# Kernel tuning notes

Hardware: AMD Instinct MI355X
Metric: run time of the kernel (lower is better)

## Reference

```python
import jax, jax.numpy as jnp
import numpy as np

B, SEQ, I_TSIZE, H, N_LAYERS = 512, 256, 64, 512, 2
E_CONST = 2.7183


def setup_inputs() -> dict:
    key = jax.random.key(0)
    ks = jax.random.split(key, 16)
    feats = jax.random.normal(ks[0], (B, SEQ, I_TSIZE - 1), dtype=jnp.float32)
    dt = jax.random.uniform(ks[1], (B, SEQ, 1), dtype=jnp.float32)  # elapsed time >= 0
    inputs_t = jnp.concatenate([feats, dt], axis=-1)  # [B, SEQ, I_TSIZE]
    i_size = I_TSIZE - 1
    inp = {"inputs_t": inputs_t}
    in_dims = [i_size, H]
    for l in range(N_LAYERS):
        c_inp = in_dims[l]
        s = 1.0 / np.sqrt(c_inp + H)
        inp[f"W{l}"] = jax.random.normal(ks[2 + 4 * l], (4 * H, c_inp + H), dtype=jnp.float32) * s
        inp[f"b{l}"] = jax.random.normal(ks[3 + 4 * l], (4 * H,), dtype=jnp.float32) * s
        sd = 1.0 / np.sqrt(H)
        inp[f"Wd{l}"] = jax.random.normal(ks[4 + 4 * l], (H, H), dtype=jnp.float32) * sd
        inp[f"bd{l}"] = jax.random.normal(ks[5 + 4 * l], (H,), dtype=jnp.float32) * sd
    return inp


def _tlstm_layer(curr_inp, W, b, Wd, bd):
    # curr_inp: [B, SEQ, feat+1] (last channel = dt). Scan over REVERSED time,
    # as in the torch loop `for t_seq in reversed(range(seq_l))`.
    batch = curr_inp.shape[0]
    h0 = jnp.zeros((batch, H), dtype=curr_inp.dtype)
    c0 = jnp.zeros((batch, H), dtype=curr_inp.dtype)

    def step(carry, xt):
        h, c = carry
        x, dt = xt[:, :-1], xt[:, -1:]
        T = 1.0 / jnp.log(dt + E_CONST)          # [B,1], broadcasts over H
        C_ST = jnp.tanh(h @ Wd.T + bd)
        h = h - C_ST + T * C_ST                  # time-decay correction
        z = jnp.concatenate([x, h], axis=1) @ W.T + b  # [B, 4H]
        ci, cf, co, cg = jnp.split(z, 4, axis=1)
        c_next = jax.nn.sigmoid(cf) * c + jax.nn.sigmoid(ci) * jnp.tanh(cg)
        h_next = jax.nn.sigmoid(co) * jnp.tanh(c_next)
        return (h_next, c_next), h_next

    xs = jnp.swapaxes(curr_inp[:, ::-1, :], 0, 1)  # [SEQ, B, feat+1], reversed time
    (h, c), hs = jax.lax.scan(step, (h0, c0), xs)
    # hs is in reversed-time order, matching torch's stack of output_inner
    layer_out = jnp.swapaxes(hs, 0, 1)  # [B, SEQ, H]
    return h, layer_out


def reference(inputs_t, W0, b0, Wd0, bd0, W1, b1, Wd1, bd1):
    t = inputs_t[..., -1:]  # [B, SEQ, 1], forward time order (as in torch code)
    params = [(W0, b0, Wd0, bd0), (W1, b1, Wd1, bd1)]
    curr = inputs_t
    h = None
    for (W, b, Wd, bd) in params:
        h, layer_out = _tlstm_layer(curr, W, b, Wd, bd)
        # NOTE: layer_out is in reversed time order but t is forward order;
        # this faithfully reproduces the original module's concatenation.
        curr = jnp.concatenate([layer_out, t], axis=-1)
    return h
```

## Files before the change

### kernel.cpp

```cpp
#include <hip/hip_runtime.h>
#include <stdint.h>

#define B_    512
#define SEQ_  256
#define H_    512
#define NSEQH (SEQ_ * H_)
#define NBLK  256
#define NTHR  (NBLK * 256)

using f32x4 = __attribute__((ext_vector_type(4))) float;
using s16x8 = __attribute__((ext_vector_type(8))) short;

#define WAITVM(N) asm volatile("s_waitcnt vmcnt(" #N ")" ::: "memory")
#define SBAR()    asm volatile("s_barrier" ::: "memory")

__device__ inline unsigned short f2bf(float f) {
  union { float f; uint32_t u; } x; x.f = f;
  uint32_t u = x.u;
  uint32_t r = u + 0x7fffu + ((u >> 16) & 1u);
  return (unsigned short)(r >> 16);
}
__device__ inline float bf2f(unsigned short h) {
  union { float f; uint32_t u; } x; x.u = ((uint32_t)h) << 16;
  return x.f;
}
__device__ inline float h2f(unsigned short u) {
  _Float16 h; __builtin_memcpy(&h, &u, 2); return (float)h;
}
__device__ inline unsigned short f2h(float f) {
  _Float16 h = (_Float16)f; unsigned short u; __builtin_memcpy(&u, &h, 2); return u;
}
__device__ inline float sigf(float x) { return 1.0f / (1.0f + expf(-x)); }

__device__ inline void gload16(const void* g, void* l) {
  __builtin_amdgcn_global_load_lds(
      (const __attribute__((address_space(1))) void*)g,
      (__attribute__((address_space(3))) void*)l, 16, 0, 0);
}
__device__ inline void gload16c(const void* g, void* l) {
  __builtin_amdgcn_global_load_lds(
      (const __attribute__((address_space(1))) void*)g,
      (__attribute__((address_space(3))) void*)l, 16, 0, 17);
}

__device__ __forceinline__ unsigned short ldh_coh(const unsigned short* p) {
  return __hip_atomic_load(p, __ATOMIC_RELAXED, __HIP_MEMORY_SCOPE_SYSTEM);
}
__device__ __forceinline__ void sth_coh(short* p, unsigned short v) {
  __hip_atomic_store((unsigned short*)p, v, __ATOMIC_RELAXED, __HIP_MEMORY_SCOPE_SYSTEM);
}

__device__ __forceinline__ void gbar_heavy(unsigned* bar) {
  __syncthreads();
  if (threadIdx.x == 0) {
    unsigned g = __hip_atomic_load(bar + 1, __ATOMIC_RELAXED, __HIP_MEMORY_SCOPE_AGENT);
    unsigned a = __hip_atomic_fetch_add(bar, 1u, __ATOMIC_ACQ_REL, __HIP_MEMORY_SCOPE_AGENT);
    if (a == (unsigned)(NBLK - 1)) {
      __hip_atomic_store(bar, 0u, __ATOMIC_RELAXED, __HIP_MEMORY_SCOPE_AGENT);
      __hip_atomic_store(bar + 1, g + 1u, __ATOMIC_RELEASE, __HIP_MEMORY_SCOPE_AGENT);
    } else {
      while (__hip_atomic_load(bar + 1, __ATOMIC_ACQUIRE, __HIP_MEMORY_SCOPE_AGENT) == g)
        __builtin_amdgcn_s_sleep(2);
    }
  }
  __syncthreads();
}

__device__ __forceinline__ void flag_signal(unsigned* f) {
  WAITVM(0);
  __syncthreads();
  if (threadIdx.x == 0)
    __hip_atomic_fetch_add(f, 1u, __ATOMIC_RELAXED, __HIP_MEMORY_SCOPE_SYSTEM);
}
__device__ __forceinline__ void flag_wait(unsigned* f, unsigned target) {
  if (threadIdx.x == 0 && target) {
    while (__hip_atomic_load(f, __ATOMIC_RELAXED, __HIP_MEMORY_SCOPE_SYSTEM) < target)
      __builtin_amdgcn_s_sleep(1);
  }
  __syncthreads();
}

__global__ void fill_kernel(float* __restrict__ out, int n, float v) {
  int i = blockIdx.x * blockDim.x + threadIdx.x;
  if (i < n) out[i] = v;
}

__device__ int compute_slot(const int* xcdmap, int myblk) {
  int cnt[8] = {0,0,0,0,0,0,0,0};
  int rank = -1;
  for (int b = 0; b < NBLK; ++b) {
    int x = xcdmap[b] & 7;
    int r = cnt[x]++;
    if (b == myblk) rank = r;
  }
  int myx = xcdmap[myblk] & 7;
  if (rank < 32) return myx * 32 + rank;
  int spill_idx = 0;
  {
    int c2[8] = {0,0,0,0,0,0,0,0};
    for (int b = 0; b < myblk; ++b) {
      int x = xcdmap[b] & 7;
      if (c2[x]++ >= 32) ++spill_idx;
    }
  }
  int k = 0;
  for (int g = 0; g < 8; ++g) {
    int filled = cnt[g] < 32 ? cnt[g] : 32;
    for (int rr = filled; rr < 32; ++rr) {
      if (k == spill_idx) return g * 32 + rr;
      ++k;
    }
  }
  return 0;
}

template<bool CVT>
__device__ __forceinline__ void g1_phase(
    char* LDS, int m0, int n0,
    const short* hhi, const short* hlo,
    const short* Wds, const float* bd, const float* tm1,
    short* huhi, short* hulo,
    const unsigned short* lo0_t, short* xhhi, short* xhlo)
{
  const int tid = threadIdx.x;
  const int w = tid >> 6, l = tid & 63;
  const int sr = tid >> 3;
  const int scs = (tid & 7) ^ (sr & 7);

  auto stage = [&](int kt) {
    char* base = LDS + (kt & 3) * 16384;
    const int kb = kt << 6;
    const size_t aoff = (size_t)(m0 + sr) * H_ + kb + scs * 8;
    gload16c(hhi + aoff, base + w * 1024);
    gload16c(hlo + aoff, base + 4096 + w * 1024);
    const size_t boff = (size_t)(n0 + sr) * 1024 + kb + scs * 8;
    gload16(Wds + boff,       base + 8192  + w * 1024);
    gload16(Wds + boff + 512, base + 12288 + w * 1024);
  };

  stage(0); stage(1); stage(2);

  const int wm = w & 1, wn = w >> 1;
  const int ar = wm * 16 + (l & 15);
  const int br = wn * 16 + (l & 15);
  const int koff = (l >> 4) * 16;
  const int aswz = (ar & 7) << 4;
  const int bswz = (br & 7) << 4;

  f32x4 acc = {0.f, 0.f, 0.f, 0.f};

  for (int kt = 0; kt < 8; ++kt) {
    if (kt < 6)       WAITVM(8);
    else if (kt == 6) WAITVM(4);
    else              WAITVM(0);
    SBAR();
    if (kt + 3 < 8) stage(kt + 3);
    char* base = LDS + (kt & 3) * 16384;
#pragma unroll
    for (int k2 = 0; k2 < 2; ++k2) {
      const int ao = (ar * 128 + k2 * 64 + koff) ^ aswz;
      const int bo = (br * 128 + k2 * 64 + koff) ^ bswz;
      s16x8 a_hi = *(const s16x8*)(base + ao);
      s16x8 a_lo = *(const s16x8*)(base + 4096 + ao);
      s16x8 b_hi = *(const s16x8*)(base + 8192 + bo);
      s16x8 b_lo = *(const s16x8*)(base + 12288 + bo);
      acc = __builtin_amdgcn_mfma_f32_16x16x32_bf16(a_hi, b_hi, acc, 0, 0, 0);
      acc = __builtin_amdgcn_mfma_f32_16x16x32_bf16(a_lo, b_hi, acc, 0, 0, 0);
      acc = __builtin_amdgcn_mfma_f32_16x16x32_bf16(a_hi, b_lo, acc, 0, 0, 0);
    }
  }

  const int n_abs = n0 + wn * 16 + (l & 15);
  const int mbase = m0 + wm * 16 + (l >> 4) * 4;
  const float bv = bd[n_abs];
#pragma unroll
  for (int r = 0; r < 4; ++r) {
    const int m_abs = mbase + r;
    const size_t off = (size_t)m_abs * H_ + n_abs;
    float cst = tanhf(acc[r] + bv);
    float hv = bf2f(ldh_coh((const unsigned short*)hhi + off)) +
               bf2f(ldh_coh((const unsigned short*)hlo + off));
    float hu = hv + tm1[m_abs] * cst;
    unsigned short hi = f2bf(hu);
    sth_coh(huhi + off, hi);
    sth_coh(hulo + off, f2bf(hu - bf2f(hi)));
    if (CVT) {
      float xv = h2f(ldh_coh(lo0_t + (size_t)m_abs * NSEQH + n_abs));
      unsigned short xh = f2bf(xv);
      sth_coh(xhhi + off, xh);
      sth_coh(xhlo + off, f2bf(xv - bf2f(xh)));
    }
  }
}

template<int K, int XK, int XSTR, bool STORE_LO0, bool XCOH>
__device__ __forceinline__ void g2_phase(
    char* LDS, int m0, int j0,
    const short* xhi, const short* xlo,
    const short* huhi, const short* hulo,
    const short* Wsp, const float* bias,
    f32x4& cv, short* hhi, short* hlo,
    unsigned short* lo0_t)
{
  constexpr int NT = K / 64;
  constexpr int KPS = 2 * K;
  const int tid = threadIdx.x;
  const int w = tid >> 6, l = tid & 63;

  auto stage = [&](int kt) {
    char* base = LDS + 65536 + (kt & 1) * 32768;
    const int kb = kt << 6;
#pragma unroll
    for (int j = 0; j < 2; ++j) {
      const int s = tid + j * 256;
      const int r = s >> 3;
      const int cs = (s & 7) ^ (r & 7);
      char* dhi = base + j * 4096 + w * 1024;
      char* dlo = base + 8192 + j * 4096 + w * 1024;
      if (kb < XK) {
        const size_t aoff = (size_t)(m0 + r) * XSTR + kb + cs * 8;
        if (XCOH) { gload16c(xhi + aoff, dhi); gload16c(xlo + aoff, dlo); }
        else      { gload16 (xhi + aoff, dhi); gload16 (xlo + aoff, dlo); }
      } else {
        const size_t aoff = (size_t)(m0 + r) * H_ + (kb - XK) + cs * 8;
        gload16c(huhi + aoff, dhi);
        gload16c(hulo + aoff, dlo);
      }
      const int src_n = (r >> 4) * H_ + j0 + (r & 15);
      const size_t boff = (size_t)src_n * KPS + kb + cs * 8;
      gload16(Wsp + boff,     base + 16384 + j * 4096 + w * 1024);
      gload16(Wsp + boff + K, base + 24576 + j * 4096 + w * 1024);
    }
  };

  stage(0); stage(1);

  const int ar = w * 16 + (l & 15);
  const int swz_a = (ar & 7) << 4;
  const int koff = (l >> 4) * 16;

  f32x4 acc[4];
#pragma unroll
  for (int i = 0; i < 4; ++i) acc[i] = (f32x4){0.f, 0.f, 0.f, 0.f};

  for (int kt = 0; kt < NT; ++kt) {
    if (kt + 1 < NT) WAITVM(8);
    else             WAITVM(0);
    SBAR();
    char* base = LDS + 65536 + (kt & 1) * 32768;
#pragma unroll
    for (int k2 = 0; k2 < 2; ++k2) {
      const int ao = (ar * 128 + k2 * 64 + koff) ^ swz_a;
      s16x8 a_hi = *(const s16x8*)(base + ao);
      s16x8 a_lo = *(const s16x8*)(base + 8192 + ao);
#pragma unroll
      for (int nf = 0; nf < 4; ++nf) {
        const int br = nf * 16 + (l & 15);
        const int bo = (br * 128 + k2 * 64 + koff) ^ ((br & 7) << 4);
        s16x8 b_hi = *(const s16x8*)(base + 16384 + bo);
        s16x8 b_lo = *(const s16x8*)(base + 24576 + bo);
        acc[nf] = __builtin_amdgcn_mfma_f32_16x16x32_bf16(a_hi, b_hi, acc[nf], 0, 0, 0);
        acc[nf] = __builtin_amdgcn_mfma_f32_16x16x32_bf16(a_lo, b_hi, acc[nf], 0, 0, 0);
        acc[nf] = __builtin_amdgcn_mfma_f32_16x16x32_bf16(a_hi, b_lo, acc[nf], 0, 0, 0);
      }
    }
    SBAR();
    if (kt + 2 < NT) stage(kt + 2);
  }

  const int j_abs = j0 + (l & 15);
  const float bi  = bias[j_abs];
  const float bfv = bias[H_ + j_abs];
  const float bo  = bias[2 * H_ + j_abs];
  const float bg  = bias[3 * H_ + j_abs];
  const int mbase = m0 + w * 16 + (l >> 4) * 4;
#pragma unroll
  for (int r = 0; r < 4; ++r) {
    const int m_abs = mbase + r;
    float zi = acc[0][r] + bi;
    float zf = acc[1][r] + bfv;
    float zo = acc[2][r] + bo;
    float zg = acc[3][r] + bg;
    float cn = sigf(zf) * cv[r] + sigf(zi) * tanhf(zg);
    float hn = sigf(zo) * tanhf(cn);
    cv[r] = cn;
    const size_t off = (size_t)m_abs * H_ + j_abs;
    unsigned short hi = f2bf(hn);
    sth_coh(hhi + off, hi);
    sth_coh(hlo + off, f2bf(hn - bf2f(hi)));
    if (STORE_LO0)
      sth_coh((short*)(lo0_t + (size_t)m_abs * NSEQH + j_abs), f2h(hn));
  }
}

__global__ __launch_bounds__(256, 1) void persist(
    const float* inputs,
    const float* W0, const float* b0, const float* Wd0, const float* bd0,
    const float* W1, const float* b1, const float* Wd1, const float* bd1,
    float* out,
    unsigned short* lo0, short* xinhi, short* xinlo,
    short* hhi, short* hlo, short* huhi, short* hulo,
    short* xhhi, short* xhlo,
    float* Tm1T, short* Wd0s, short* Wd1s, short* W0s, short* W1s,
    unsigned* bar, int* xcdmap)
{
  __shared__ __align__(16) char LDS[131072];
  const int gtid = blockIdx.x * 256 + threadIdx.x;

  if (threadIdx.x == 0) {
    unsigned xcc;
    asm volatile("s_getreg_b32 %0, hwreg(20, 0, 32)" : "=s"(xcc));
    xcdmap[blockIdx.x] = (int)(xcc & 7u);
  }

  auto dosplit = [&](const float* W, short* Ws, int N, int Ksrc, int Kpad, int pad_at) {
    const int total = N * Kpad;
    for (int idx = gtid; idx < total; idx += NTHR) {
      int n = idx / Kpad, c = idx - n * Kpad;
      int sc = c;
      if (pad_at >= 0) { if (c == pad_at) sc = -1; else if (c > pad_at) sc = c - 1; }
      float v = 0.f;
      if (sc >= 0 && sc < Ksrc) v = W[(size_t)n * Ksrc + sc];
      unsigned short hi = f2bf(v);
      unsigned short lo = f2bf(v - bf2f(hi));
      size_t base = (size_t)n * (2 * Kpad);
      Ws[base + c]        = (short)hi;
      Ws[base + Kpad + c] = (short)lo;
    }
  };
  dosplit(Wd0, Wd0s, 512, 512, 512, -1);
  dosplit(Wd1, Wd1s, 512, 512, 512, -1);
  dosplit(W0, W0s, 2048, 575, 576, 63);
  dosplit(W1, W1s, 2048, 1024, 1024, -1);
  for (int idx = gtid; idx < B_ * SEQ_ * 64; idx += NTHR) {
    float v = inputs[idx];
    unsigned short hi = f2bf(v);
    xinhi[idx] = (short)hi;
    xinlo[idx] = (short)f2bf(v - bf2f(hi));
  }
  for (int idx = gtid; idx < B_ * SEQ_; idx += NTHR) {
    int b = idx / SEQ_, t = idx - b * SEQ_;
    float dt = inputs[(size_t)b * (SEQ_ * 64) + t * 64 + 63];
    Tm1T[t * B_ + b] = 1.0f / logf(dt + 2.7183f) - 1.0f;
  }
  for (int idx = gtid; idx < B_ * H_; idx += NTHR) {
    hhi[idx] = 0; hlo[idx] = 0;
  }
  gbar_heavy(bar);

  const int myw = compute_slot(xcdmap, blockIdx.x);
  const int wg = myw >> 5, rr = myw & 31;
  const int g1_n0 = (wg * 2 + (rr & 1)) * 32;
  const int g1_m0 = (rr >> 1) * 32;
  const int g2_j0 = (wg * 4 + (rr & 3)) * 16;
  const int g2_m0 = (rr >> 2) * 64;

  const int t = rr >> 2;
  const int cid = wg * 4 + (rr & 3);
  unsigned* g1d = bar + 512 + t * 32;
  unsigned* g2d = bar + 768 + t * 32;
  unsigned* zd  = bar + 256 + t * 32;

  for (int layer = 0; layer < 2; ++layer) {
    f32x4 cv = {0.f, 0.f, 0.f, 0.f};
    if (layer == 1) {
      flag_wait(g2d, 32u * SEQ_);
      const size_t base = (size_t)t * 64 * H_;
      for (int i = cid * 256 + threadIdx.x; i < 64 * H_; i += 32 * 256) {
        sth_coh(hhi + base + i, 0); sth_coh(hlo + base + i, 0);
      }
      flag_signal(zd);
      flag_wait(zd, 32u);
    }
    for (int s = 0; s < SEQ_; ++s) {
      const unsigned ss = (unsigned)(layer * SEQ_ + s);
      const int torig = SEQ_ - 1 - s;
      flag_wait(g2d, 32u * ss);
      if (layer == 0)
        g1_phase<false>(LDS, g1_m0, g1_n0, hhi, hlo, Wd0s, bd0,
                        Tm1T + (size_t)torig * B_, huhi, hulo,
                        nullptr, nullptr, nullptr);
      else
        g1_phase<true>(LDS, g1_m0, g1_n0, hhi, hlo, Wd1s, bd1,
                       Tm1T + (size_t)torig * B_, huhi, hulo,
                       lo0 + (size_t)torig * H_, xhhi, xhlo);
      flag_signal(g1d);
      flag_wait(g1d, 32u * (ss + 1));
      if (layer == 0)
        g2_phase<576, 64, SEQ_ * 64, true, false>(
            LDS, g2_m0, g2_j0,
            xinhi + (size_t)torig * 64, xinlo + (size_t)torig * 64,
            huhi, hulo, W0s, b0, cv, hhi, hlo,
            lo0 + (size_t)s * H_);
      else
        g2_phase<1024, 512, H_, false, true>(
            LDS, g2_m0, g2_j0,
            xhhi, xhlo, huhi, hulo, W1s, b1,
            cv, hhi, hlo, nullptr);
      flag_signal(g2d);
    }
  }

  flag_wait(g2d, 32u * (unsigned)(2 * SEQ_));
  {
    const size_t base = (size_t)t * 64 * H_;
    for (int i = cid * 256 + threadIdx.x; i < 64 * H_; i += 32 * 256)
      out[base + i] = bf2f(ldh_coh((const unsigned short*)hhi + base + i)) +
                      bf2f(ldh_coh((const unsigned short*)hlo + base + i));
  }
}

extern "C" void kernel_launch(void* const* d_in, const int* in_sizes, int n_in,
                              void* d_out, int out_size, void* d_ws, size_t ws_size,
                              hipStream_t stream) {
  const float* inputs = (const float*)d_in[0];
  const float* W0  = (const float*)d_in[1];
  const float* b0  = (const float*)d_in[2];
  const float* Wd0 = (const float*)d_in[3];
  const float* bd0 = (const float*)d_in[4];
  const float* W1  = (const float*)d_in[5];
  const float* b1  = (const float*)d_in[6];
  const float* Wd1 = (const float*)d_in[7];
  const float* bd1 = (const float*)d_in[8];

  char* ws = (char*)d_ws;
  size_t off = 0;
  auto alloc = [&](size_t bytes) -> char* {
    char* p = ws + off;
    off += (bytes + 1023) & ~(size_t)1023;
    return p;
  };
  unsigned* bar = (unsigned*)alloc(4096);
  int* xcdmap = (int*)alloc(NBLK * 4);
  unsigned short* lo0 = (unsigned short*)alloc((size_t)B_ * SEQ_ * H_ * 2);
  short* xinhi = (short*)alloc((size_t)B_ * SEQ_ * 64 * 2);
  short* xinlo = (short*)alloc((size_t)B_ * SEQ_ * 64 * 2);
  short* hhi   = (short*)alloc((size_t)B_ * H_ * 2);
  short* hlo   = (short*)alloc((size_t)B_ * H_ * 2);
  short* huhi  = (short*)alloc((size_t)B_ * H_ * 2);
  short* hulo  = (short*)alloc((size_t)B_ * H_ * 2);
  short* xhhi  = (short*)alloc((size_t)B_ * H_ * 2);
  short* xhlo  = (short*)alloc((size_t)B_ * H_ * 2);
  float* Tm1T  = (float*)alloc((size_t)SEQ_ * B_ * 4);
  short* Wd0s  = (short*)alloc((size_t)512 * 1024 * 2);
  short* Wd1s  = (short*)alloc((size_t)512 * 1024 * 2);
  short* W0s   = (short*)alloc((size_t)2048 * 1152 * 2);
  short* W1s   = (short*)alloc((size_t)2048 * 2048 * 2);

  if (off > ws_size) {
    fill_kernel<<<(out_size + 255) / 256, 256, 0, stream>>>(
        (float*)d_out, out_size, (float)(ws_size >> 20));
    return;
  }

  hipMemsetAsync(bar, 0, 4096, stream);
  persist<<<NBLK, 256, 0, stream>>>(
      inputs, W0, b0, Wd0, bd0, W1, b1, Wd1, bd1,
      (float*)d_out,
      lo0, xinhi, xinlo,
      hhi, hlo, huhi, hulo, xhhi, xhlo,
      Tm1T, Wd0s, Wd1s, W0s, W1s, bar, xcdmap);
}
```

Before: 9.248 ms.

## Reshape gate GEMM tile to 32 rows by 32 hidden units per block

The recurrent gate GEMM phase now gives each block a 32-row by 32-hidden-unit tile (128 gate columns) instead of 64 rows by 16 units. The four waves are arranged 2x2 over rows and hidden halves, and the LDS staging buffers are rebased to offset 0 and resized to match. This makes the gate phase's block-to-row mapping match the first GEMM phase, likely to cut cross-block dependency and wait time between phases. In exchange each block loads more bytes per k-step, since the weight tile doubles while the activation tile halves. The rebased LDS region may also overlap storage used elsewhere in the kernel.

New measurement: 9.784 ms. 5.8% more time.

```diff
diff --git a/kernel.cpp b/kernel.cpp
--- a/kernel.cpp
+++ b/kernel.cpp
@@ -208,15 +208,13 @@
   const int w = tid >> 6, l = tid & 63;
 
   auto stage = [&](int kt) {
-    char* base = LDS + 65536 + (kt & 1) * 32768;
+    char* base = LDS + (kt & 1) * 40960;
     const int kb = kt << 6;
-#pragma unroll
-    for (int j = 0; j < 2; ++j) {
-      const int s = tid + j * 256;
-      const int r = s >> 3;
-      const int cs = (s & 7) ^ (r & 7);
-      char* dhi = base + j * 4096 + w * 1024;
-      char* dlo = base + 8192 + j * 4096 + w * 1024;
+    {
+      const int r = tid >> 3;
+      const int cs = (tid & 7) ^ (r & 7);
+      char* dhi = base + w * 1024;
+      char* dlo = base + 4096 + w * 1024;
       if (kb < XK) {
         const size_t aoff = (size_t)(m0 + r) * XSTR + kb + cs * 8;
         if (XCOH) { gload16c(xhi + aoff, dhi); gload16c(xlo + aoff, dlo); }
@@ -226,17 +224,24 @@
         gload16c(huhi + aoff, dhi);
         gload16c(hulo + aoff, dlo);
       }
-      const int src_n = (r >> 4) * H_ + j0 + (r & 15);
-      const size_t boff = (size_t)src_n * KPS + kb + cs * 8;
-      gload16(Wsp + boff,     base + 16384 + j * 4096 + w * 1024);
-      gload16(Wsp + boff + K, base + 24576 + j * 4096 + w * 1024);
+    }
+#pragma unroll
+    for (int q = 0; q < 4; ++q) {
+      const int s = tid + q * 256;
+      const int r2 = s >> 3;
+      const int cs2 = (s & 7) ^ (r2 & 7);
+      const int src_n = (r2 >> 5) * H_ + j0 + (r2 & 31);
+      const size_t boff = (size_t)src_n * KPS + kb + cs2 * 8;
+      gload16(Wsp + boff,     base + 8192  + q * 4096 + w * 1024);
+      gload16(Wsp + boff + K, base + 24576 + q * 4096 + w * 1024);
     }
   };
 
   stage(0); stage(1);
 
-  const int ar = w * 16 + (l & 15);
-  const int swz_a = (ar & 7) << 4;
+  const int mf = w & 1, jh = w >> 1;
+  const int ar = mf * 16 + (l & 15);
+  const int aswz = (ar & 7) << 4;
   const int koff = (l >> 4) * 16;
 
   f32x4 acc[4];
@@ -244,36 +249,36 @@
   for (int i = 0; i < 4; ++i) acc[i] = (f32x4){0.f, 0.f, 0.f, 0.f};
 
   for (int kt = 0; kt < NT; ++kt) {
-    if (kt + 1 < NT) WAITVM(8);
+    if (kt + 1 < NT) WAITVM(10);
     else             WAITVM(0);
     SBAR();
-    char* base = LDS + 65536 + (kt & 1) * 32768;
+    char* base = LDS + (kt & 1) * 40960;
 #pragma unroll
     for (int k2 = 0; k2 < 2; ++k2) {
-      const int ao = (ar * 128 + k2 * 64 + koff) ^ swz_a;
+      const int ao = (ar * 128 + k2 * 64 + koff) ^ aswz;
       s16x8 a_hi = *(const s16x8*)(base + ao);
-      s16x8 a_lo = *(const s16x8*)(base + 8192 + ao);
-#pragma unroll
-      for (int nf = 0; nf < 4; ++nf) {
-        const int br = nf * 16 + (l & 15);
+      s16x8 a_lo = *(const s16x8*)(base + 4096 + ao);
+#pragma unroll
+      for (int g = 0; g < 4; ++g) {
+        const int br = g * 32 + jh * 16 + (l & 15);
         const int bo = (br * 128 + k2 * 64 + koff) ^ ((br & 7) << 4);
-        s16x8 b_hi = *(const s16x8*)(base + 16384 + bo);
+        s16x8 b_hi = *(const s16x8*)(base + 8192 + bo);
         s16x8 b_lo = *(const s16x8*)(base + 24576 + bo);
-        acc[nf] = __builtin_amdgcn_mfma_f32_16x16x32_bf16(a_hi, b_hi, acc[nf], 0, 0, 0);
-        acc[nf] = __builtin_amdgcn_mfma_f32_16x16x32_bf16(a_lo, b_hi, acc[nf], 0, 0, 0);
-        acc[nf] = __builtin_amdgcn_mfma_f32_16x16x32_bf16(a_hi, b_lo, acc[nf], 0, 0, 0);
+        acc[g] = __builtin_amdgcn_mfma_f32_16x16x32_bf16(a_hi, b_hi, acc[g], 0, 0, 0);
+        acc[g] = __builtin_amdgcn_mfma_f32_16x16x32_bf16(a_lo, b_hi, acc[g], 0, 0, 0);
+        acc[g] = __builtin_amdgcn_mfma_f32_16x16x32_bf16(a_hi, b_lo, acc[g], 0, 0, 0);
       }
     }
     SBAR();
     if (kt + 2 < NT) stage(kt + 2);
   }
 
-  const int j_abs = j0 + (l & 15);
+  const int j_abs = j0 + jh * 16 + (l & 15);
   const float bi  = bias[j_abs];
   const float bfv = bias[H_ + j_abs];
   const float bo  = bias[2 * H_ + j_abs];
   const float bg  = bias[3 * H_ + j_abs];
-  const int mbase = m0 + w * 16 + (l >> 4) * 4;
+  const int mbase = m0 + mf * 16 + (l >> 4) * 4;
 #pragma unroll
   for (int r = 0; r < 4; ++r) {
     const int m_abs = mbase + r;
@@ -352,8 +357,8 @@
   const int wg = myw >> 5, rr = myw & 31;
   const int g1_n0 = (wg * 2 + (rr & 1)) * 32;
   const int g1_m0 = (rr >> 1) * 32;
-  const int g2_j0 = (wg * 4 + (rr & 3)) * 16;
-  const int g2_m0 = (rr >> 2) * 64;
+  const int g2_j0 = (wg * 2 + (rr & 1)) * 32;
+  const int g2_m0 = (rr >> 1) * 32;
 
   const int t = rr >> 2;
   const int cid = wg * 4 + (rr & 3);
```
